# Optimization experiments

Hardware: AMD Instinct MI355X
Metric: run time of the kernel (lower is better)

## Reference

```python
import jax, jax.numpy as jnp
import numpy as np

C_S = 1024
H = 16
M = 1  # num_vector_messages
B, S = 2, 1024
SQRT3 = 3.0 ** 0.5
LN_EPS = 1e-5


def setup_inputs() -> dict:
    key = jax.random.key(0)
    ks = jax.random.split(key, 8)
    s = jax.random.normal(ks[0], (B, S, C_S), dtype=jnp.float32)
    # random proper-ish frames: orthonormalize random 3x3 via QR
    A = jax.random.normal(ks[1], (B, S, 3, 3), dtype=jnp.float32)
    rot, _ = jnp.linalg.qr(A)
    trans = jax.random.normal(ks[2], (B, S, 3), dtype=jnp.float32)
    affine_mask = jnp.ones((B, S), dtype=bool)
    sequence_id = jax.random.randint(ks[3], (B, S), 0, 4, dtype=jnp.int32)
    chain_id = jax.random.randint(ks[4], (B, S), 0, 4, dtype=jnp.int32)
    dim_proj = 4 * H * 3 + H * 3 * M
    ln_w = jnp.ones((C_S,), dtype=jnp.float32)
    w_proj = jax.random.normal(ks[5], (dim_proj, C_S), dtype=jnp.float32) / np.sqrt(C_S)
    w_out = jax.random.normal(ks[6], (C_S, H * 3 * M), dtype=jnp.float32) / np.sqrt(H * 3 * M)
    dist_scale = jnp.zeros((H,), dtype=jnp.float32)
    rot_scale = jnp.zeros((H,), dtype=jnp.float32)
    return {"s": s, "rot": rot, "trans": trans, "ln_w": ln_w, "w_proj": w_proj,
            "w_out": w_out, "dist_scale": dist_scale, "rot_scale": rot_scale,
            "affine_mask": affine_mask, "sequence_id": sequence_id, "chain_id": chain_id}


def reference(s, rot, trans, ln_w, w_proj, w_out, dist_scale, rot_scale,
              affine_mask, sequence_id, chain_id):
    b, n, c = s.shape
    h, m = H, M
    NEG = jnp.finfo(s.dtype).min
    # attention bias: 1.0 for same-sequence pairs, -inf for invalid frames / cross-chain
    seq_eq = (sequence_id[:, :, None] == sequence_id[:, None, :]).astype(s.dtype)
    bias = seq_eq[:, None]  # [b,1,s,s]
    bias = jnp.where(affine_mask[:, None, None, :], bias, NEG)
    chain_diff = chain_id[:, :, None] != chain_id[:, None, :]
    bias = jnp.where(chain_diff[:, None], NEG, bias)
    # LayerNorm (no bias)
    mu = jnp.mean(s, axis=-1, keepdims=True)
    var = jnp.var(s, axis=-1, keepdims=True)
    ns = (s - mu) / jnp.sqrt(var + LN_EPS) * ln_w
    p = jnp.einsum('bsc,dc->bsd', ns, w_proj)
    n_rot = h * 2 * 3 + h * 3 * m
    vec_rot = p[..., :n_rot].reshape(b, n, 2 * h + h * m, 3)
    vec_dist = p[..., n_rot:].reshape(b, n, 2 * h, 3)
    # rotate into global frame; dist vectors also translated
    rot_vecs = jnp.einsum('bsij,bshj->bshi', rot, vec_rot)
    q_rot, k_rot, value = rot_vecs[:, :, :h], rot_vecs[:, :, h:2 * h], rot_vecs[:, :, 2 * h:]
    dist_vecs = jnp.einsum('bsij,bshj->bshi', rot, vec_dist) + trans[:, :, None, :]
    q_dist, k_dist = dist_vecs[:, :, :h], dist_vecs[:, :, h:]
    # distance term [b,h,q,k]
    qd = q_dist.transpose(0, 2, 1, 3)  # b h s 3
    kd = k_dist.transpose(0, 2, 1, 3)
    diff = qd[:, :, :, None, :] - kd[:, :, None, :, :]
    distance_term = jnp.sqrt(jnp.sum(diff * diff, axis=-1)) / SQRT3
    rotation_term = jnp.einsum('bqhd,bkhd->bhqk', q_rot, k_rot) / SQRT3
    dw = jax.nn.softplus(dist_scale)[None, :, None, None]
    rw = jax.nn.softplus(rot_scale)[None, :, None, None]
    attn = rotation_term * rw - distance_term * dw + bias
    attn = jax.nn.softmax(attn, axis=-1)
    # value: b s (h m) 3 -> b h s (m 3)
    v = value.reshape(b, n, h, m, 3).transpose(0, 2, 1, 3, 4).reshape(b, h, n, m * 3)
    out = jnp.einsum('bhqk,bhkd->bhqd', attn, v)
    out = out.reshape(b, h, n, m, 3).transpose(0, 2, 1, 3, 4).reshape(b, n, h * m, 3)
    out = jnp.einsum('bsji,bshj->bshi', rot, out)  # inverse rotation R^T
    out = out.reshape(b, n, h * m * 3)
    out = jnp.where(affine_mask[..., None], out, 0.0)
    return jnp.einsum('bsd,cd->bsc', out, w_out)
```

## Files before the change

kernel.cpp:

```cpp
#include <hip/hip_runtime.h>
#include <math.h>

#define NB 2
#define NS 1024
#define NC 1024
#define NH 16
#define DIMP 240
#define KSPLIT 16
#define AKH 16

constexpr float INV_SQRT3 = 0.57735026919f;

__global__ __launch_bounds__(256) void pre_kernel(const float* __restrict__ s,
                                                  const float* __restrict__ lnw,
                                                  float* __restrict__ ns,
                                                  const float* __restrict__ wp,
                                                  float* __restrict__ wt) {
    __shared__ float sh[64 * 61];
    int tid = threadIdx.x;
    if (blockIdx.x < NB * NS) {
        int row = blockIdx.x;
        const float4* sp = (const float4*)(s + (size_t)row * NC);
        float4 v = sp[tid];
        float sum = v.x + v.y + v.z + v.w;
        float sq  = v.x*v.x + v.y*v.y + v.z*v.z + v.w*v.w;
        #pragma unroll
        for (int off = 32; off; off >>= 1) {
            sum += __shfl_down(sum, off);
            sq  += __shfl_down(sq, off);
        }
        float* s1 = sh; float* s2 = sh + 4;
        int wave = tid >> 6;
        if ((tid & 63) == 0) { s1[wave] = sum; s2[wave] = sq; }
        __syncthreads();
        float tot   = s1[0] + s1[1] + s1[2] + s1[3];
        float totsq = s2[0] + s2[1] + s2[2] + s2[3];
        float mu  = tot * (1.0f / NC);
        float var = totsq * (1.0f / NC) - mu * mu;
        float rstd = rsqrtf(var + 1e-5f);
        float4 w = ((const float4*)lnw)[tid];
        float4 o;
        o.x = (v.x - mu) * rstd * w.x;
        o.y = (v.y - mu) * rstd * w.y;
        o.z = (v.z - mu) * rstd * w.z;
        o.w = (v.w - mu) * rstd * w.w;
        ((float4*)(ns + (size_t)row * NC))[tid] = o;
    } else {
        int bx = blockIdx.x - NB * NS;
        int k0 = (bx & 15) * 64;
        int d0 = (bx >> 4) * 60;
        float (*T)[61] = (float (*)[61])sh;
        #pragma unroll
        for (int i = 0; i < 15; i++) {
            int idx = i * 256 + tid;
            int dd = idx >> 6, kk = idx & 63;
            T[kk][dd] = wp[(size_t)(d0 + dd) * NC + k0 + kk];
        }
        __syncthreads();
        #pragma unroll
        for (int i = 0; i < 15; i++) {
            int idx = i * 256 + tid;
            int kk = idx / 60, dd = idx % 60;
            wt[(size_t)(k0 + kk) * DIMP + d0 + dd] = T[kk][dd];
        }
    }
}

__global__ __launch_bounds__(256) void proj_kernel(const float* __restrict__ ns,
                                                   const float* __restrict__ wt,
                                                   float* __restrict__ pp,
                                                   int use_atomic) {
    int tid = threadIdx.x;
    int wave = tid >> 6, lane = tid & 63;
    int row0 = blockIdx.x * 32;
    int ky = blockIdx.y;
    int k0 = ky * 64;

    __shared__ float A[32][64];
    #pragma unroll
    for (int i = 0; i < 2; i++) {
        int idx = tid + i * 256;
        int r = idx >> 4, c4 = idx & 15;
        *(float4*)&A[r][c4 * 4] = *(const float4*)(ns + (size_t)(row0 + r) * NC + k0 + c4 * 4);
    }
    __syncthreads();

    int wr0 = wave * 8;
    int c0 = lane * 4;
    bool active = c0 < DIMP;
    int c0m = active ? c0 : (DIMP - 4);
    const float* wb = wt + (size_t)k0 * DIMP + c0m;

    float acc[8][4];
    #pragma unroll
    for (int r = 0; r < 8; r++)
        #pragma unroll
        for (int c = 0; c < 4; c++) acc[r][c] = 0.0f;

    float4 wa[4], wx[4];
    #pragma unroll
    for (int j = 0; j < 4; j++) wa[j] = *(const float4*)(wb + (size_t)j * DIMP);

    for (int g = 0; g < 16; g += 2) {
        #pragma unroll
        for (int j = 0; j < 4; j++)
            wx[j] = *(const float4*)(wb + (size_t)((g + 1) * 4 + j) * DIMP);
        #pragma unroll
        for (int r = 0; r < 8; r++) {
            float4 a4 = *(const float4*)&A[wr0 + r][g * 4];
            #pragma unroll
            for (int c = 0; c < 4; c++) {
                float* ac = &acc[r][c];
                *ac = fmaf(a4.x, ((const float*)&wa[0])[c], *ac);
                *ac = fmaf(a4.y, ((const float*)&wa[1])[c], *ac);
                *ac = fmaf(a4.z, ((const float*)&wa[2])[c], *ac);
                *ac = fmaf(a4.w, ((const float*)&wa[3])[c], *ac);
            }
        }
        int kn2 = (g + 2 < 16) ? (g + 2) * 4 : 0;
        #pragma unroll
        for (int j = 0; j < 4; j++)
            wa[j] = *(const float4*)(wb + (size_t)(kn2 + j) * DIMP);
        #pragma unroll
        for (int r = 0; r < 8; r++) {
            float4 a4 = *(const float4*)&A[wr0 + r][(g + 1) * 4];
            #pragma unroll
            for (int c = 0; c < 4; c++) {
                float* ac = &acc[r][c];
                *ac = fmaf(a4.x, ((const float*)&wx[0])[c], *ac);
                *ac = fmaf(a4.y, ((const float*)&wx[1])[c], *ac);
                *ac = fmaf(a4.z, ((const float*)&wx[2])[c], *ac);
                *ac = fmaf(a4.w, ((const float*)&wx[3])[c], *ac);
            }
        }
    }
    if (active) {
        if (use_atomic) {
            #pragma unroll
            for (int r = 0; r < 8; r++)
                #pragma unroll
                for (int c = 0; c < 4; c++)
                    atomicAdd(&pp[(size_t)(row0 + wr0 + r) * DIMP + c0 + c], acc[r][c]);
        } else {
            float* dst = pp + (size_t)ky * (NB * NS * DIMP);
            #pragma unroll
            for (int r = 0; r < 8; r++)
                *(float4*)(dst + (size_t)(row0 + wr0 + r) * DIMP + c0) =
                    make_float4(acc[r][0], acc[r][1], acc[r][2], acc[r][3]);
        }
    }
}

__global__ __launch_bounds__(256) void build_kernel(const float* __restrict__ pp, int nred,
                                                    const float* __restrict__ rot,
                                                    const float* __restrict__ trans,
                                                    const float* __restrict__ dist_scale,
                                                    const float* __restrict__ rot_scale,
                                                    const int* __restrict__ seq,
                                                    const int* __restrict__ chain,
                                                    const int* __restrict__ amask,
                                                    float4* __restrict__ qrb,
                                                    float4* __restrict__ qdb,
                                                    float4* __restrict__ kp) {
    int gid = blockIdx.x * 256 + threadIdx.x;
    if (gid >= NB * NS * 80) return;
    int j  = gid % 80;
    int bs = gid / 80;
    int b  = bs >> 10;
    int si = bs & 1023;
    int off = (j < 48) ? 3 * j : 144 + 3 * (j - 48);
    float vx = 0.0f, vy = 0.0f, vz = 0.0f;
    for (int ky = 0; ky < nred; ky++) {
        const float* pr = pp + (size_t)ky * (NB * NS * DIMP) + (size_t)bs * DIMP + off;
        vx += pr[0]; vy += pr[1]; vz += pr[2];
    }
    const float* R = rot + (size_t)bs * 9;
    float ox = R[0] * vx + R[1] * vy + R[2] * vz;
    float oy = R[3] * vx + R[4] * vy + R[5] * vz;
    float oz = R[6] * vx + R[7] * vy + R[8] * vz;
    if (j >= 48) {
        ox += trans[(size_t)bs * 3 + 0];
        oy += trans[(size_t)bs * 3 + 1];
        oz += trans[(size_t)bs * 3 + 2];
    }
    if (j < 16) {
        float sc = log1pf(__expf(rot_scale[j])) * INV_SQRT3;
        qrb[(size_t)(b * NH + j) * NS + si] = make_float4(ox * sc, oy * sc, oz * sc, 0.0f);
    } else if (j < 32) {
        int h = j - 16;
        float ck = (float)chain[bs] + 1000.0f * (float)(1 - amask[bs]);
        kp[((size_t)(b * NH + h) * NS + si) * 3 + 0] = make_float4(ox, oy, oz, ck);
    } else if (j < 48) {
        int h = j - 32;
        kp[((size_t)(b * NH + h) * NS + si) * 3 + 2] = make_float4(ox, oy, oz, 0.0f);
    } else if (j < 64) {
        int h = j - 48;
        float sc = log1pf(__expf(dist_scale[h])) * INV_SQRT3;
        qdb[(size_t)(b * NH + h) * NS + si] = make_float4(ox * sc, oy * sc, oz * sc, 0.0f);
    } else {
        int h = j - 64;
        float sc = log1pf(__expf(dist_scale[h])) * INV_SQRT3;
        kp[((size_t)(b * NH + h) * NS + si) * 3 + 1] =
            make_float4(ox * sc, oy * sc, oz * sc, (float)seq[bs]);
    }
}

__global__ __launch_bounds__(256) void attn_kernel(
    const float4* __restrict__ qrb, const float4* __restrict__ qdb,
    const float4* __restrict__ kp,
    float4* __restrict__ pacc) {
    __shared__ float4 kS[192];
    int bx = blockIdx.x;
    int ks = bx & (AKH - 1), qc = (bx >> 4) & 3, bh = bx >> 6;
    int tid = threadIdx.x;
    int q = qc * 256 + tid;
    int base = bh * NS;
    const float4* kb = kp + (size_t)base * 3;

    if (tid < 192) kS[tid] = kb[(size_t)ks * 192 + tid];
    __syncthreads();

    float4 a = qrb[base + q];
    float4 d = qdb[base + q];
    float cq = kb[(size_t)q * 3 + 0].w;
    float sq = kb[(size_t)q * 3 + 1].w;

    float l = 0.0f, ax = 0.0f, ay = 0.0f, az = 0.0f;
    #pragma unroll 4
    for (int j = 0; j < 64; j++) {
        float4 f0 = kS[j * 3 + 0];
        float4 f1 = kS[j * 3 + 1];
        float4 f2 = kS[j * 3 + 2];
        float rt = fmaf(a.x, f0.x, fmaf(a.y, f0.y, a.z * f0.z));
        float dx = d.x - f1.x, dy = d.y - f1.y, dz = d.z - f1.z;
        float dist = sqrtf(fmaf(dx, dx, fmaf(dy, dy, dz * dz)));
        float dc = f0.w - cq;
        float arg = fmaf(-100.0f, fabsf(dc), rt - dist) +
                    ((f1.w == sq) ? -15.0f : -16.0f);
        float pw = __expf(arg);
        l += pw;
        ax = fmaf(pw, f2.x, ax);
        ay = fmaf(pw, f2.y, ay);
        az = fmaf(pw, f2.z, az);
    }
    pacc[(size_t)ks * (32 * NS) + base + q] = make_float4(ax, ay, az, l);
}

__global__ __launch_bounds__(256) void attnfin_kernel(const float4* __restrict__ pacc,
                                                      const float4* __restrict__ kp,
                                                      const float* __restrict__ rot,
                                                      float* __restrict__ small) {
    int i = blockIdx.x * 256 + threadIdx.x;
    int bh = i >> 10, q = i & 1023;
    int b = bh >> 4, h = bh & 15;
    float4 s = make_float4(0.0f, 0.0f, 0.0f, 0.0f);
    #pragma unroll
    for (int j = 0; j < AKH; j++) {
        float4 t = pacc[(size_t)j * (32 * NS) + i];
        s.x += t.x; s.y += t.y; s.z += t.z; s.w += t.w;
    }
    float inv = 1.0f / s.w;
    float ox = s.x * inv, oy = s.y * inv, oz = s.z * inv;
    const float* R = rot + (size_t)(b * NS + q) * 9;
    float wx = R[0] * ox + R[3] * oy + R[6] * oz;
    float wy = R[1] * ox + R[4] * oy + R[7] * oz;
    float wz = R[2] * ox + R[5] * oy + R[8] * oz;
    float cq = kp[((size_t)bh * NS + q) * 3 + 0].w;
    if (cq >= 500.0f) { wx = 0; wy = 0; wz = 0; }
    float* o = small + (size_t)(b * NS + q) * 48 + h * 3;
    o[0] = wx; o[1] = wy; o[2] = wz;
}

__global__ __launch_bounds__(256) void outgemm_kernel(const float* __restrict__ small,
                                                      const float* __restrict__ wout,
                                                      float* __restrict__ out) {
    int c  = blockIdx.y * 256 + threadIdx.x;
    int r0 = blockIdx.x * 16;
    __shared__ float sm[16][48];
    for (int i = threadIdx.x; i < 16 * 48; i += 256)
        sm[i / 48][i % 48] = small[(size_t)(r0 + i / 48) * 48 + i % 48];
    __syncthreads();
    float w[48];
    #pragma unroll
    for (int d = 0; d < 48; d += 4) {
        float4 t = *(const float4*)(wout + (size_t)c * 48 + d);
        w[d] = t.x; w[d + 1] = t.y; w[d + 2] = t.z; w[d + 3] = t.w;
    }
    #pragma unroll 4
    for (int r = 0; r < 16; r++) {
        float acc = 0.0f;
        #pragma unroll
        for (int d = 0; d < 48; d++) acc = fmaf(w[d], sm[r][d], acc);
        out[(size_t)(r0 + r) * NC + c] = acc;
    }
}

extern "C" void kernel_launch(void* const* d_in, const int* in_sizes, int n_in,
                              void* d_out, int out_size, void* d_ws, size_t ws_size,
                              hipStream_t stream) {
    const float* s     = (const float*)d_in[0];
    const float* rot   = (const float*)d_in[1];
    const float* trans = (const float*)d_in[2];
    const float* lnw   = (const float*)d_in[3];
    const float* wproj = (const float*)d_in[4];
    const float* wout  = (const float*)d_in[5];
    const float* dsc   = (const float*)d_in[6];
    const float* rsc   = (const float*)d_in[7];
    const int* amask   = (const int*)d_in[8];
    const int* seq     = (const int*)d_in[9];
    const int* chain   = (const int*)d_in[10];
    float* out = (float*)d_out;

    float* ns = (float*)d_ws;
    float4* qrb = (float4*)(ns + (size_t)NB * NS * NC);
    float4* qdb = qrb + (size_t)NB * NH * NS;
    float4* kpk = qdb + (size_t)NB * NH * NS;
    float* small = (float*)(kpk + (size_t)3 * NB * NH * NS);
    float* pp = small + (size_t)NB * NS * 48;
    float* wt = (float*)qrb;
    float4* pacc = (float4*)pp;

    size_t need = ((char*)(pp + (size_t)KSPLIT * NB * NS * DIMP)) - (char*)d_ws;
    int use_atomic = (ws_size < need) ? 1 : 0;

    pre_kernel<<<NB * NS + 64, 256, 0, stream>>>(s, lnw, ns, wproj, wt);
    if (use_atomic) {
        hipMemsetAsync(pp, 0, (size_t)NB * NS * DIMP * sizeof(float), stream);
        proj_kernel<<<dim3(64, KSPLIT), 256, 0, stream>>>(ns, wt, pp, 1);
        build_kernel<<<(NB * NS * 80 + 255) / 256, 256, 0, stream>>>(pp, 1, rot, trans, dsc, rsc,
                                                                     seq, chain, amask, qrb, qdb, kpk);
    } else {
        proj_kernel<<<dim3(64, KSPLIT), 256, 0, stream>>>(ns, wt, pp, 0);
        build_kernel<<<(NB * NS * 80 + 255) / 256, 256, 0, stream>>>(pp, KSPLIT, rot, trans, dsc, rsc,
                                                                     seq, chain, amask, qrb, qdb, kpk);
    }
    attn_kernel<<<NB * NH * 4 * AKH, 256, 0, stream>>>(qrb, qdb, kpk, pacc);
    attnfin_kernel<<<NB * NH * NS / 256, 256, 0, stream>>>(pacc, kpk, rot, small);
    outgemm_kernel<<<dim3(NB * NS / 16, 4), 256, 0, stream>>>(small, wout, out);
}
```

Measured before the change: 154.3 us.

## Fuse LayerNorm apply into projection, merge attention finalize with output GEMM

The pre kernel now computes only per-row mean and rstd (one wave per row), and the projection kernel normalizes s on the fly while loading its tile. This avoids writing and re-reading the normalized activation buffer. The attention finalize and output GEMM are merged into one kernel, which drops the intermediate small buffer and one launch. The attention inner loop switches to exp2 with log2e folded into the scales and biases, and uses the raw hardware sqrt. In exchange, the projection now re-reads s and the stats once per K-split block, and the fused output kernel loops over all 1024 output columns per block.

Result: faster. 150.2 us (-2.6%).

```diff
diff --git a/kernel.cpp b/kernel.cpp
--- a/kernel.cpp
+++ b/kernel.cpp
@@ -10,43 +10,39 @@
 #define AKH 16
 
 constexpr float INV_SQRT3 = 0.57735026919f;
+constexpr float LOG2E     = 1.44269504089f;
+constexpr float BIAS0     = -23.0831169f;
+constexpr float BIAS1     = -21.6404252f;
 
 __global__ __launch_bounds__(256) void pre_kernel(const float* __restrict__ s,
-                                                  const float* __restrict__ lnw,
-                                                  float* __restrict__ ns,
+                                                  float2* __restrict__ stats,
                                                   const float* __restrict__ wp,
                                                   float* __restrict__ wt) {
     __shared__ float sh[64 * 61];
     int tid = threadIdx.x;
-    if (blockIdx.x < NB * NS) {
-        int row = blockIdx.x;
+    if (blockIdx.x < NB * NS / 4) {
+        int wave = tid >> 6, lane = tid & 63;
+        int row = blockIdx.x * 4 + wave;
         const float4* sp = (const float4*)(s + (size_t)row * NC);
-        float4 v = sp[tid];
-        float sum = v.x + v.y + v.z + v.w;
-        float sq  = v.x*v.x + v.y*v.y + v.z*v.z + v.w*v.w;
+        float sum = 0.0f, sq = 0.0f;
+        #pragma unroll
+        for (int i = 0; i < 4; i++) {
+            float4 v = sp[i * 64 + lane];
+            sum += v.x + v.y + v.z + v.w;
+            sq  += v.x * v.x + v.y * v.y + v.z * v.z + v.w * v.w;
+        }
         #pragma unroll
         for (int off = 32; off; off >>= 1) {
             sum += __shfl_down(sum, off);
             sq  += __shfl_down(sq, off);
         }
-        float* s1 = sh; float* s2 = sh + 4;
-        int wave = tid >> 6;
-        if ((tid & 63) == 0) { s1[wave] = sum; s2[wave] = sq; }
-        __syncthreads();
-        float tot   = s1[0] + s1[1] + s1[2] + s1[3];
-        float totsq = s2[0] + s2[1] + s2[2] + s2[3];
-        float mu  = tot * (1.0f / NC);
-        float var = totsq * (1.0f / NC) - mu * mu;
-        float rstd = rsqrtf(var + 1e-5f);
-        float4 w = ((const float4*)lnw)[tid];
-        float4 o;
-        o.x = (v.x - mu) * rstd * w.x;
-        o.y = (v.y - mu) * rstd * w.y;
-        o.z = (v.z - mu) * rstd * w.z;
-        o.w = (v.w - mu) * rstd * w.w;
-        ((float4*)(ns + (size_t)row * NC))[tid] = o;
+        if (lane == 0) {
+            float mu  = sum * (1.0f / NC);
+            float var = sq * (1.0f / NC) - mu * mu;
+            stats[row] = make_float2(mu, rsqrtf(var + 1e-5f));
+        }
     } else {
-        int bx = blockIdx.x - NB * NS;
+        int bx = blockIdx.x - NB * NS / 4;
         int k0 = (bx & 15) * 64;
         int d0 = (bx >> 4) * 60;
         float (*T)[61] = (float (*)[61])sh;
@@ -66,7 +62,9 @@
     }
 }
 
-__global__ __launch_bounds__(256) void proj_kernel(const float* __restrict__ ns,
+__global__ __launch_bounds__(256) void proj_kernel(const float* __restrict__ s,
+                                                   const float2* __restrict__ stats,
+                                                   const float* __restrict__ lnw,
                                                    const float* __restrict__ wt,
                                                    float* __restrict__ pp,
                                                    int use_atomic) {
@@ -81,7 +79,15 @@
     for (int i = 0; i < 2; i++) {
         int idx = tid + i * 256;
         int r = idx >> 4, c4 = idx & 15;
-        *(float4*)&A[r][c4 * 4] = *(const float4*)(ns + (size_t)(row0 + r) * NC + k0 + c4 * 4);
+        float4 v = *(const float4*)(s + (size_t)(row0 + r) * NC + k0 + c4 * 4);
+        float2 st = stats[row0 + r];
+        float4 w = *(const float4*)(lnw + k0 + c4 * 4);
+        float4 o;
+        o.x = (v.x - st.x) * st.y * w.x;
+        o.y = (v.y - st.x) * st.y * w.y;
+        o.z = (v.z - st.x) * st.y * w.z;
+        o.w = (v.w - st.x) * st.y * w.w;
+        *(float4*)&A[r][c4 * 4] = o;
     }
     __syncthreads();
 
@@ -184,7 +190,7 @@
         oz += trans[(size_t)bs * 3 + 2];
     }
     if (j < 16) {
-        float sc = log1pf(__expf(rot_scale[j])) * INV_SQRT3;
+        float sc = log1pf(__expf(rot_scale[j])) * INV_SQRT3 * LOG2E;
         qrb[(size_t)(b * NH + j) * NS + si] = make_float4(ox * sc, oy * sc, oz * sc, 0.0f);
     } else if (j < 32) {
         int h = j - 16;
@@ -195,11 +201,11 @@
         kp[((size_t)(b * NH + h) * NS + si) * 3 + 2] = make_float4(ox, oy, oz, 0.0f);
     } else if (j < 64) {
         int h = j - 48;
-        float sc = log1pf(__expf(dist_scale[h])) * INV_SQRT3;
+        float sc = log1pf(__expf(dist_scale[h])) * INV_SQRT3 * LOG2E;
         qdb[(size_t)(b * NH + h) * NS + si] = make_float4(ox * sc, oy * sc, oz * sc, 0.0f);
     } else {
         int h = j - 64;
-        float sc = log1pf(__expf(dist_scale[h])) * INV_SQRT3;
+        float sc = log1pf(__expf(dist_scale[h])) * INV_SQRT3 * LOG2E;
         kp[((size_t)(b * NH + h) * NS + si) * 3 + 1] =
             make_float4(ox * sc, oy * sc, oz * sc, (float)seq[bs]);
     }
@@ -233,11 +239,11 @@
         float4 f2 = kS[j * 3 + 2];
         float rt = fmaf(a.x, f0.x, fmaf(a.y, f0.y, a.z * f0.z));
         float dx = d.x - f1.x, dy = d.y - f1.y, dz = d.z - f1.z;
-        float dist = sqrtf(fmaf(dx, dx, fmaf(dy, dy, dz * dz)));
+        float dist = __builtin_amdgcn_sqrtf(fmaf(dx, dx, fmaf(dy, dy, dz * dz)));
         float dc = f0.w - cq;
         float arg = fmaf(-100.0f, fabsf(dc), rt - dist) +
-                    ((f1.w == sq) ? -15.0f : -16.0f);
-        float pw = __expf(arg);
+                    ((f1.w == sq) ? BIAS1 : BIAS0);
+        float pw = exp2f(arg);
         l += pw;
         ax = fmaf(pw, f2.x, ax);
         ay = fmaf(pw, f2.y, ay);
@@ -246,52 +252,54 @@
     pacc[(size_t)ks * (32 * NS) + base + q] = make_float4(ax, ay, az, l);
 }
 
-__global__ __launch_bounds__(256) void attnfin_kernel(const float4* __restrict__ pacc,
-                                                      const float4* __restrict__ kp,
-                                                      const float* __restrict__ rot,
-                                                      float* __restrict__ small) {
-    int i = blockIdx.x * 256 + threadIdx.x;
-    int bh = i >> 10, q = i & 1023;
-    int b = bh >> 4, h = bh & 15;
-    float4 s = make_float4(0.0f, 0.0f, 0.0f, 0.0f);
-    #pragma unroll
-    for (int j = 0; j < AKH; j++) {
-        float4 t = pacc[(size_t)j * (32 * NS) + i];
-        s.x += t.x; s.y += t.y; s.z += t.z; s.w += t.w;
-    }
-    float inv = 1.0f / s.w;
-    float ox = s.x * inv, oy = s.y * inv, oz = s.z * inv;
-    const float* R = rot + (size_t)(b * NS + q) * 9;
-    float wx = R[0] * ox + R[3] * oy + R[6] * oz;
-    float wy = R[1] * ox + R[4] * oy + R[7] * oz;
-    float wz = R[2] * ox + R[5] * oy + R[8] * oz;
-    float cq = kp[((size_t)bh * NS + q) * 3 + 0].w;
-    if (cq >= 500.0f) { wx = 0; wy = 0; wz = 0; }
-    float* o = small + (size_t)(b * NS + q) * 48 + h * 3;
-    o[0] = wx; o[1] = wy; o[2] = wz;
-}
-
-__global__ __launch_bounds__(256) void outgemm_kernel(const float* __restrict__ small,
-                                                      const float* __restrict__ wout,
-                                                      float* __restrict__ out) {
-    int c  = blockIdx.y * 256 + threadIdx.x;
-    int r0 = blockIdx.x * 16;
-    __shared__ float sm[16][48];
-    for (int i = threadIdx.x; i < 16 * 48; i += 256)
-        sm[i / 48][i % 48] = small[(size_t)(r0 + i / 48) * 48 + i % 48];
+__global__ __launch_bounds__(256) void finout_kernel(const float4* __restrict__ pacc,
+                                                     const float4* __restrict__ kp,
+                                                     const float* __restrict__ rot,
+                                                     const float* __restrict__ wout,
+                                                     float* __restrict__ out) {
+    __shared__ float sm[8][48];
+    int tid = threadIdx.x;
+    int r0 = blockIdx.x * 8;
+    if (tid < 128) {
+        int r = tid & 7, h = tid >> 3;
+        int bq = r0 + r;
+        int b = bq >> 10, q = bq & 1023;
+        int i = (b * NH + h) * NS + q;
+        float sx = 0.0f, sy = 0.0f, sz = 0.0f, sw = 0.0f;
+        #pragma unroll
+        for (int j = 0; j < AKH; j++) {
+            float4 t = pacc[(size_t)j * (NB * NH * NS) + i];
+            sx += t.x; sy += t.y; sz += t.z; sw += t.w;
+        }
+        float inv = 1.0f / sw;
+        float ox = sx * inv, oy = sy * inv, oz = sz * inv;
+        const float* R = rot + (size_t)bq * 9;
+        float wxv = R[0] * ox + R[3] * oy + R[6] * oz;
+        float wyv = R[1] * ox + R[4] * oy + R[7] * oz;
+        float wzv = R[2] * ox + R[5] * oy + R[8] * oz;
+        float cq = kp[(size_t)i * 3].w;
+        if (cq >= 500.0f) { wxv = 0; wyv = 0; wzv = 0; }
+        sm[r][h * 3 + 0] = wxv;
+        sm[r][h * 3 + 1] = wyv;
+        sm[r][h * 3 + 2] = wzv;
+    }
     __syncthreads();
-    float w[48];
-    #pragma unroll
-    for (int d = 0; d < 48; d += 4) {
-        float4 t = *(const float4*)(wout + (size_t)c * 48 + d);
-        w[d] = t.x; w[d + 1] = t.y; w[d + 2] = t.z; w[d + 3] = t.w;
-    }
-    #pragma unroll 4
-    for (int r = 0; r < 16; r++) {
-        float acc = 0.0f;
-        #pragma unroll
-        for (int d = 0; d < 48; d++) acc = fmaf(w[d], sm[r][d], acc);
-        out[(size_t)(r0 + r) * NC + c] = acc;
+    #pragma unroll 1
+    for (int ch = 0; ch < 4; ch++) {
+        int c = ch * 256 + tid;
+        float w[48];
+        #pragma unroll
+        for (int d = 0; d < 48; d += 4) {
+            float4 t = *(const float4*)(wout + (size_t)c * 48 + d);
+            w[d] = t.x; w[d + 1] = t.y; w[d + 2] = t.z; w[d + 3] = t.w;
+        }
+        #pragma unroll 4
+        for (int r = 0; r < 8; r++) {
+            float acc = 0.0f;
+            #pragma unroll
+            for (int d = 0; d < 48; d++) acc = fmaf(w[d], sm[r][d], acc);
+            out[(size_t)(r0 + r) * NC + c] = acc;
+        }
     }
 }
 
@@ -311,30 +319,28 @@
     const int* chain   = (const int*)d_in[10];
     float* out = (float*)d_out;
 
-    float* ns = (float*)d_ws;
-    float4* qrb = (float4*)(ns + (size_t)NB * NS * NC);
+    float2* stats = (float2*)d_ws;
+    float4* qrb = (float4*)((float*)d_ws + 4096);
     float4* qdb = qrb + (size_t)NB * NH * NS;
     float4* kpk = qdb + (size_t)NB * NH * NS;
-    float* small = (float*)(kpk + (size_t)3 * NB * NH * NS);
-    float* pp = small + (size_t)NB * NS * 48;
+    float* pp = (float*)(kpk + (size_t)3 * NB * NH * NS);
     float* wt = (float*)qrb;
     float4* pacc = (float4*)pp;
 
     size_t need = ((char*)(pp + (size_t)KSPLIT * NB * NS * DIMP)) - (char*)d_ws;
     int use_atomic = (ws_size < need) ? 1 : 0;
 
-    pre_kernel<<<NB * NS + 64, 256, 0, stream>>>(s, lnw, ns, wproj, wt);
+    pre_kernel<<<NB * NS / 4 + 64, 256, 0, stream>>>(s, stats, wproj, wt);
     if (use_atomic) {
         hipMemsetAsync(pp, 0, (size_t)NB * NS * DIMP * sizeof(float), stream);
-        proj_kernel<<<dim3(64, KSPLIT), 256, 0, stream>>>(ns, wt, pp, 1);
+        proj_kernel<<<dim3(64, KSPLIT), 256, 0, stream>>>(s, stats, lnw, wt, pp, 1);
         build_kernel<<<(NB * NS * 80 + 255) / 256, 256, 0, stream>>>(pp, 1, rot, trans, dsc, rsc,
                                                                      seq, chain, amask, qrb, qdb, kpk);
     } else {
-        proj_kernel<<<dim3(64, KSPLIT), 256, 0, stream>>>(ns, wt, pp, 0);
+        proj_kernel<<<dim3(64, KSPLIT), 256, 0, stream>>>(s, stats, lnw, wt, pp, 0);
         build_kernel<<<(NB * NS * 80 + 255) / 256, 256, 0, stream>>>(pp, KSPLIT, rot, trans, dsc, rsc,
                                                                      seq, chain, amask, qrb, qdb, kpk);
     }
     attn_kernel<<<NB * NH * 4 * AKH, 256, 0, stream>>>(qrb, qdb, kpk, pacc);
-    attnfin_kernel<<<NB * NH * NS / 256, 256, 0, stream>>>(pacc, kpk, rot, small);
-    outgemm_kernel<<<dim3(NB * NS / 16, 4), 256, 0, stream>>>(small, wout, out);
-}
+    finout_kernel<<<NB * NS / 8, 256, 0, stream>>>(pacc, kpk, rot, wout, out);
+}
```
